# Kernel tuning notes

Measured on AMD Instinct MI355X. Metric: run time of the kernel, lower is better.

## Reference

```python
import jax, jax.numpy as jnp
import numpy as np

B, S, H, L, NH, T, V = 16, 512, 768, 6, 12, 32, 10000


def setup_inputs() -> dict:
    key = jax.random.key(0)
    ks = jax.random.split(key, 16)
    p = lambda i, shape: jax.random.normal(ks[i], shape, jnp.float32) * 0.02
    return {
        "input_ids": jax.random.randint(ks[0], (B, S), 0, V),
        "labels": jax.random.randint(ks[1], (B, S), 0, T),
        "if_crf": 1,
        "emb": p(2, (V, H)),
        "attn_in_w": p(3, (L, 3 * H, H)), "attn_in_b": p(4, (L, 3 * H)),
        "attn_out_w": p(5, (L, H, H)), "attn_out_b": p(6, (L, H)),
        "ln1_g": jnp.ones((L, H), jnp.float32), "ln1_b": jnp.zeros((L, H), jnp.float32),
        "ln2_g": jnp.ones((L, H), jnp.float32), "ln2_b": jnp.zeros((L, H), jnp.float32),
        "ffn_w1": p(7, (L, H, H)), "ffn_b1": p(8, (L, H)),
        "ffn_w2": p(9, (L, H, H)), "ffn_b2": p(10, (L, H)),
        "head_w": p(11, (T, H)), "head_b": p(12, (T,)),
        "crf_start": p(13, (T,)), "crf_end": p(14, (T,)), "crf_trans": p(15, (T, T)),
    }


def _layer_norm(x, g, b, eps=1e-5):
    m = x.mean(-1, keepdims=True)
    v = ((x - m) ** 2).mean(-1, keepdims=True)
    return (x - m) * jax.lax.rsqrt(v + eps) * g + b


def _encoder(x, params):
    # PyTorch post-norm TransformerEncoderLayer, batch_first, relu, dropout=0 (eval)
    def layer(x, p):
        in_w, in_b, out_w, out_b, g1, b1, g2, b2, w1, bb1, w2, bb2 = p
        Bq, Sq, Hq = x.shape
        dh = Hq // NH
        qkv = x @ in_w.T + in_b                       # [B,S,3H]
        q, k, v = jnp.split(qkv, 3, axis=-1)
        q = q.reshape(Bq, Sq, NH, dh).transpose(0, 2, 1, 3)
        k = k.reshape(Bq, Sq, NH, dh).transpose(0, 2, 1, 3)
        v = v.reshape(Bq, Sq, NH, dh).transpose(0, 2, 1, 3)
        scale = 1.0 / np.sqrt(dh).astype(np.float32).item()
        a = jax.nn.softmax(jnp.einsum('bhqd,bhkd->bhqk', q, k) * scale, axis=-1)
        o = jnp.einsum('bhqk,bhkd->bhqd', a, v).transpose(0, 2, 1, 3).reshape(Bq, Sq, Hq)
        o = o @ out_w.T + out_b
        x = _layer_norm(x + o, g1, b1)
        ff = jax.nn.relu(x @ w1.T + bb1) @ w2.T + bb2
        x = _layer_norm(x + ff, g2, b2)
        return x, None
    x, _ = jax.lax.scan(layer, x, params)
    return x


def _crf_llh(emis, tags, start, end, trans):
    # torchcrf log-likelihood, no mask, reduction='sum'
    Bq = emis.shape[0]
    emit = jnp.take_along_axis(emis, tags[:, :, None], axis=2)[:, :, 0].sum(1)   # [B]
    tr = trans[tags[:, :-1], tags[:, 1:]].sum(1)                                 # [B]
    num = start[tags[:, 0]] + emit + tr + end[tags[:, -1]]
    # partition via forward algorithm (scan over time)
    def step(score, e_t):  # score [B,T], e_t [B,T]
        ns = jax.nn.logsumexp(score[:, :, None] + trans[None], axis=1) + e_t
        return ns, None
    score0 = start[None] + emis[:, 0]
    scoreN, _ = jax.lax.scan(step, score0, jnp.swapaxes(emis, 0, 1)[1:])
    logZ = jax.nn.logsumexp(scoreN + end[None], axis=1)
    return (num - logZ).sum()


def _viterbi(emis, start, end, trans):
    score0 = start[None] + emis[:, 0]
    def step(score, e_t):
        cand = score[:, :, None] + trans[None]   # [B,T,T]
        return cand.max(1) + e_t, cand.argmax(1)
    scoreN, hist = jax.lax.scan(step, score0, jnp.swapaxes(emis, 0, 1)[1:])  # hist [S-1,B,T]
    last = (scoreN + end[None]).argmax(1)  # [B]
    def back(tag, h_t):
        prev = jnp.take_along_axis(h_t, tag[:, None], axis=1)[:, 0]
        return prev, prev
    _, prevs = jax.lax.scan(back, last, hist, reverse=True)  # prevs[i] = tag at pos i
    return jnp.concatenate([prevs.T, last[:, None]], axis=1)  # [B,S]


def reference(input_ids, labels, if_crf, emb, attn_in_w, attn_in_b, attn_out_w, attn_out_b,
              ln1_g, ln1_b, ln2_g, ln2_b, ffn_w1, ffn_b1, ffn_w2, ffn_b2,
              head_w, head_b, crf_start, crf_end, crf_trans):
    x = emb[input_ids]
    params = (attn_in_w, attn_in_b, attn_out_w, attn_out_b, ln1_g, ln1_b, ln2_g, ln2_b,
              ffn_w1, ffn_b1, ffn_w2, ffn_b2)
    logits = _encoder(x, params)            # [B,S,H]
    emis = logits @ head_w.T + head_b       # [B,S,T]
    if if_crf:
        llh = _crf_llh(emis, labels, crf_start, crf_end, crf_trans)
        tags = _viterbi(emis, crf_start, crf_end, crf_trans)
        return logits, -llh / 10000.0, tags
    else:
        return logits, emis, jnp.argmax(emis, axis=-1)
```

## Files before the change

### kernel.cpp

```cpp
#include <hip/hip_runtime.h>

#define MTOK 8192
#define HD   768
#define H3   2304
#define NL   6
#define TT   32

typedef __attribute__((ext_vector_type(4))) float f32x4;
typedef __attribute__((ext_vector_type(8))) short v8bf;
typedef __attribute__((ext_vector_type(4))) unsigned short us4;
typedef __attribute__((ext_vector_type(8))) unsigned short us8;

__device__ __forceinline__ unsigned short bf16rne(float v) {
    unsigned int u = __float_as_uint(v);
    u += 0x7FFFu + ((u >> 16) & 1u);
    return (unsigned short)(u >> 16);
}
__device__ __forceinline__ float bf2f(unsigned short h) {
    return __uint_as_float(((unsigned int)h) << 16);
}
__device__ __forceinline__ unsigned int split_pack(float v) {
    unsigned short h = bf16rne(v);
    unsigned short m = bf16rne(v - bf2f(h));
    return (unsigned int)h | ((unsigned int)m << 16);
}

__device__ __forceinline__ void gload16(const unsigned short* g, unsigned short* l) {
    __builtin_amdgcn_global_load_lds(
        (const __attribute__((address_space(1))) unsigned int*)g,
        (__attribute__((address_space(3))) unsigned int*)l, 16, 0, 0);
}

__global__ __launch_bounds__(256)
void wsplit_kernel(const float* __restrict__ src, unsigned short* __restrict__ h,
                   unsigned short* __restrict__ m, int n4)
{
    int i = blockIdx.x * 256 + threadIdx.x;
    if (i >= n4) return;
    float4 v = reinterpret_cast<const float4*>(src)[i];
    us4 hv, mv; unsigned int p;
    p = split_pack(v.x); hv[0] = (unsigned short)p; mv[0] = (unsigned short)(p >> 16);
    p = split_pack(v.y); hv[1] = (unsigned short)p; mv[1] = (unsigned short)(p >> 16);
    p = split_pack(v.z); hv[2] = (unsigned short)p; mv[2] = (unsigned short)(p >> 16);
    p = split_pack(v.w); hv[3] = (unsigned short)p; mv[3] = (unsigned short)(p >> 16);
    reinterpret_cast<us4*>(h)[i] = hv;
    reinterpret_cast<us4*>(m)[i] = mv;
}

template<bool RELU, bool SPLITOUT>
__global__ __launch_bounds__(256)
void gemm_pair_kernel(const unsigned short* __restrict__ Ahg, const unsigned short* __restrict__ Amg,
                      const unsigned short* __restrict__ Bhg, const unsigned short* __restrict__ Bmg,
                      const float* __restrict__ bias, float* __restrict__ Cf,
                      unsigned short* __restrict__ Ch, unsigned short* __restrict__ Cm, int N)
{
    __shared__ unsigned short lds[4][128 * 64];
    const int tid = threadIdx.x;
    const int lane = tid & 63, wave = tid >> 6;
    const int wm = wave >> 1, wn = wave & 1;
    const int bn = blockIdx.x, bm = blockIdx.y;
    const int g = lane >> 4, lr = lane & 15;

    const int srow = lane >> 3;
    const int schunk = ((lane & 7) ^ srow) * 8;
    const size_t aoff = ((size_t)(bm * 128 + wave * 32 + srow)) * HD + schunk;
    const size_t boff = ((size_t)(bn * 128 + wave * 32 + srow)) * HD + schunk;

    f32x4 acc[4][4] = {};

    for (int kt = 0; kt < 12; ++kt) {
        __syncthreads();
        const int k64 = kt * 64;
        #pragma unroll
        for (int i = 0; i < 4; ++i) {
            const size_t ra = aoff + (size_t)i * 8 * HD + k64;
            const size_t rb = boff + (size_t)i * 8 * HD + k64;
            unsigned short* lb = (unsigned short*)&lds[0][(wave * 32 + i * 8) * 64];
            gload16(Ahg + ra, lb);
            gload16(Amg + ra, lb + 8192);
            gload16(Bhg + rb, lb + 16384);
            gload16(Bmg + rb, lb + 24576);
        }
        __syncthreads();
        #pragma unroll
        for (int kk = 0; kk < 2; ++kk) {
            v8bf ah[4], am[4], bh[4], bmv[4];
            #pragma unroll
            for (int i = 0; i < 4; ++i) {
                int row = wm * 64 + i * 16 + lr;
                int ub = row * 64 + ((((kk << 2) + g) ^ (row & 7)) << 3);
                ah[i] = *reinterpret_cast<const v8bf*>(&lds[0][ub]);
                am[i] = *reinterpret_cast<const v8bf*>(&lds[1][ub]);
            }
            #pragma unroll
            for (int i = 0; i < 4; ++i) {
                int row = wn * 64 + i * 16 + lr;
                int ub = row * 64 + ((((kk << 2) + g) ^ (row & 7)) << 3);
                bh[i]  = *reinterpret_cast<const v8bf*>(&lds[2][ub]);
                bmv[i] = *reinterpret_cast<const v8bf*>(&lds[3][ub]);
            }
            #pragma unroll
            for (int i = 0; i < 4; ++i)
                #pragma unroll
                for (int j = 0; j < 4; ++j) {
                    acc[i][j] = __builtin_amdgcn_mfma_f32_16x16x32_bf16(ah[i], bh[j],  acc[i][j], 0, 0, 0);
                    acc[i][j] = __builtin_amdgcn_mfma_f32_16x16x32_bf16(ah[i], bmv[j], acc[i][j], 0, 0, 0);
                    acc[i][j] = __builtin_amdgcn_mfma_f32_16x16x32_bf16(am[i], bh[j],  acc[i][j], 0, 0, 0);
                    acc[i][j] = __builtin_amdgcn_mfma_f32_16x16x32_bf16(am[i], bmv[j], acc[i][j], 0, 0, 0);
                }
        }
    }
    #pragma unroll
    for (int j = 0; j < 4; ++j) {
        int n = bn * 128 + wn * 64 + j * 16 + lr;
        float bv = bias[n];
        #pragma unroll
        for (int i = 0; i < 4; ++i) {
            int mr = bm * 128 + wm * 64 + i * 16 + 4 * g;
            #pragma unroll
            for (int r = 0; r < 4; ++r) {
                float y = acc[i][j][r] + bv;
                if (RELU) y = fmaxf(y, 0.0f);
                size_t idx = (size_t)(mr + r) * N + n;
                if (SPLITOUT) {
                    unsigned int pk = split_pack(y);
                    Ch[idx] = (unsigned short)pk;
                    Cm[idx] = (unsigned short)(pk >> 16);
                } else {
                    Cf[idx] = y;
                }
            }
        }
    }
}

__global__ __launch_bounds__(256)
void vtrans_kernel(const unsigned short* __restrict__ qh, const unsigned short* __restrict__ qm,
                   unsigned short* __restrict__ vth, unsigned short* __restrict__ vtm)
{
    __shared__ unsigned short Th[4096], Tm[4096];
    const int kt = blockIdx.x, bh = blockIdx.y;
    const int b = bh / 12, h = bh % 12;
    const int tid = threadIdx.x;
    #pragma unroll
    for (int is = 0; is < 2; ++is) {
        int c = is * 256 + tid;
        int r = c >> 3, dc = c & 7;
        size_t src = ((size_t)b * 512 + kt * 64 + r) * H3 + 1536 + h * 64 + dc * 8;
        int swz = (dc ^ (r & 7) ^ (r >> 3)) * 8;
        *reinterpret_cast<us8*>(&Th[r * 64 + swz]) = *reinterpret_cast<const us8*>(&qh[src]);
        *reinterpret_cast<us8*>(&Tm[r * 64 + swz]) = *reinterpret_cast<const us8*>(&qm[src]);
    }
    __syncthreads();
    #pragma unroll
    for (int is = 0; is < 2; ++is) {
        int c = is * 256 + tid;
        int d = c >> 3, rg = c & 7;
        us8 vh, vm;
        #pragma unroll
        for (int e = 0; e < 8; ++e) {
            int r = rg * 8 + e;
            int addr = r * 64 + (((d >> 3) ^ (r & 7) ^ (r >> 3)) * 8) + (d & 7);
            vh[e] = Th[addr]; vm[e] = Tm[addr];
        }
        size_t dst = ((size_t)bh * 64 + d) * 512 + kt * 64 + rg * 8;
        *reinterpret_cast<us8*>(&vth[dst]) = vh;
        *reinterpret_cast<us8*>(&vtm[dst]) = vm;
    }
}

__global__ __launch_bounds__(256, 2)
void attn_kernel(const unsigned short* __restrict__ qh, const unsigned short* __restrict__ qm,
                 const unsigned short* __restrict__ vth, const unsigned short* __restrict__ vtm,
                 unsigned short* __restrict__ ohp, unsigned short* __restrict__ omp)
{
    __shared__ unsigned short Kh[4096], Km[4096], Vh[4096], Vm[4096];
    __shared__ unsigned short Ph[4][1024], Pm[4][1024];
    const int qhalf = blockIdx.x;
    const int bh = blockIdx.y;
    const int b = bh / 12, h = bh % 12;
    const int tid = threadIdx.x, lane = tid & 63, wave = tid >> 6;
    const int g = lane >> 4, lr = lane & 15;
    const size_t rowbase = (size_t)b * 512;
    const int qbase = qhalf * 256 + wave * 64;

    v8bf aqh[4][2], aqm[4][2];
    #pragma unroll
    for (int i = 0; i < 4; ++i)
        #pragma unroll
        for (int kk = 0; kk < 2; ++kk) {
            size_t a = (rowbase + qbase + i * 16 + lr) * H3 + h * 64 + (kk * 4 + g) * 8;
            aqh[i][kk] = *reinterpret_cast<const v8bf*>(&qh[a]);
            aqm[i][kk] = *reinterpret_cast<const v8bf*>(&qm[a]);
        }

    float m_run[4][4], l_run[4][4];
    f32x4 O[4][4];
    #pragma unroll
    for (int i = 0; i < 4; ++i)
        #pragma unroll
        for (int r = 0; r < 4; ++r) {
            m_run[i][r] = -__builtin_inff(); l_run[i][r] = 0.0f;
            O[i][r] = (f32x4){0.0f, 0.0f, 0.0f, 0.0f};
        }

    const int srow = lane >> 3;
    const int schunk = ((lane & 7) ^ srow) * 8;

    for (int kt = 0; kt < 8; ++kt) {
        __syncthreads();
        #pragma unroll
        for (int is = 0; is < 2; ++is) {
            int rowg = is * 32 + wave * 8;
            size_t ksrc = (rowbase + kt * 64 + rowg + srow) * H3 + 768 + h * 64 + schunk;
            size_t vsrc = ((size_t)bh * 64 + rowg + srow) * 512 + kt * 64 + schunk;
            gload16(qh + ksrc, &Kh[rowg * 64]);
            gload16(qm + ksrc, &Km[rowg * 64]);
            gload16(vth + vsrc, &Vh[rowg * 64]);
            gload16(vtm + vsrc, &Vm[rowg * 64]);
        }
        __syncthreads();

        #pragma unroll
        for (int i = 0; i < 4; ++i) {
            f32x4 s[4] = {};
            #pragma unroll
            for (int kk = 0; kk < 2; ++kk) {
                #pragma unroll
                for (int j = 0; j < 4; ++j) {
                    int krow = j * 16 + lr;
                    int uk = krow * 64 + (((kk * 4 + g) ^ (krow & 7)) * 8);
                    v8bf bkh = *reinterpret_cast<const v8bf*>(&Kh[uk]);
                    v8bf bkm = *reinterpret_cast<const v8bf*>(&Km[uk]);
                    s[j] = __builtin_amdgcn_mfma_f32_16x16x32_bf16(aqh[i][kk], bkh, s[j], 0, 0, 0);
                    s[j] = __builtin_amdgcn_mfma_f32_16x16x32_bf16(aqh[i][kk], bkm, s[j], 0, 0, 0);
                    s[j] = __builtin_amdgcn_mfma_f32_16x16x32_bf16(aqm[i][kk], bkh, s[j], 0, 0, 0);
                }
            }
            float mnew[4], alpha[4], rsum[4];
            #pragma unroll
            for (int rr = 0; rr < 4; ++rr) {
                float t = fmaxf(fmaxf(s[0][rr], s[1][rr]), fmaxf(s[2][rr], s[3][rr])) * 0.125f;
                #pragma unroll
                for (int off = 1; off < 16; off <<= 1) t = fmaxf(t, __shfl_xor(t, off));
                mnew[rr] = fmaxf(m_run[i][rr], t);
                alpha[rr] = __expf(m_run[i][rr] - mnew[rr]);
                m_run[i][rr] = mnew[rr];
                rsum[rr] = 0.0f;
            }
            #pragma unroll
            for (int j = 0; j < 4; ++j) {
                #pragma unroll
                for (int rr = 0; rr < 4; ++rr) {
                    float p = __expf(s[j][rr] * 0.125f - mnew[rr]);
                    rsum[rr] += p;
                    int prow = 4 * g + rr;
                    int ub = prow * 64 + ((((j * 2 + (lr >> 3)) ^ (prow & 7)) << 3) | (lr & 7));
                    unsigned int pk = split_pack(p);
                    Ph[wave][ub] = (unsigned short)pk; Pm[wave][ub] = (unsigned short)(pk >> 16);
                }
            }
            #pragma unroll
            for (int rr = 0; rr < 4; ++rr) {
                float t = rsum[rr];
                #pragma unroll
                for (int off = 1; off < 16; off <<= 1) t += __shfl_xor(t, off);
                l_run[i][rr] = l_run[i][rr] * alpha[rr] + t;
                O[i][0][rr] *= alpha[rr]; O[i][1][rr] *= alpha[rr];
                O[i][2][rr] *= alpha[rr]; O[i][3][rr] *= alpha[rr];
            }
            #pragma unroll
            for (int kk = 0; kk < 2; ++kk) {
                int up = lr * 64 + (((kk * 4 + g) ^ (lr & 7)) * 8);
                v8bf aph = *reinterpret_cast<const v8bf*>(&Ph[wave][up]);
                v8bf apm = *reinterpret_cast<const v8bf*>(&Pm[wave][up]);
                #pragma unroll
                for (int j = 0; j < 4; ++j) {
                    int vrow = j * 16 + lr;
                    int uv = vrow * 64 + (((kk * 4 + g) ^ (vrow & 7)) * 8);
                    v8bf bvh = *reinterpret_cast<const v8bf*>(&Vh[uv]);
                    v8bf bvm = *reinterpret_cast<const v8bf*>(&Vm[uv]);
                    O[i][j] = __builtin_amdgcn_mfma_f32_16x16x32_bf16(aph, bvh, O[i][j], 0, 0, 0);
                    O[i][j] = __builtin_amdgcn_mfma_f32_16x16x32_bf16(aph, bvm, O[i][j], 0, 0, 0);
                    O[i][j] = __builtin_amdgcn_mfma_f32_16x16x32_bf16(apm, bvh, O[i][j], 0, 0, 0);
                }
            }
        }
    }
    #pragma unroll
    for (int i = 0; i < 4; ++i)
        #pragma unroll
        for (int j = 0; j < 4; ++j) {
            int d = j * 16 + lr;
            #pragma unroll
            for (int rr = 0; rr < 4; ++rr) {
                size_t tok = rowbase + qbase + i * 16 + 4 * g + rr;
                unsigned int pk = split_pack(O[i][j][rr] / l_run[i][rr]);
                ohp[tok * HD + h * 64 + d] = (unsigned short)pk;
                omp[tok * HD + h * 64 + d] = (unsigned short)(pk >> 16);
            }
        }
}

__global__ __launch_bounds__(256)
void ln_residual_kernel(unsigned short* __restrict__ xh, unsigned short* __restrict__ xm,
                        const float* __restrict__ t,
                        const float* __restrict__ gamma, const float* __restrict__ beta)
{
    int tok = blockIdx.x * 4 + (threadIdx.x >> 6);
    int lane = threadIdx.x & 63;
    float v[12];
    float s = 0.0f;
    #pragma unroll
    for (int j = 0; j < 12; ++j) {
        size_t c = (size_t)tok * HD + j * 64 + lane;
        v[j] = bf2f(xh[c]) + bf2f(xm[c]) + t[c];
        s += v[j];
    }
    #pragma unroll
    for (int off = 32; off; off >>= 1) s += __shfl_xor(s, off);
    float mean = s * (1.0f / 768.0f);
    float vs = 0.0f;
    #pragma unroll
    for (int j = 0; j < 12; ++j) { float d = v[j] - mean; vs += d * d; }
    #pragma unroll
    for (int off = 32; off; off >>= 1) vs += __shfl_xor(vs, off);
    float rstd = rsqrtf(vs * (1.0f / 768.0f) + 1e-5f);
    #pragma unroll
    for (int j = 0; j < 12; ++j) {
        size_t c = (size_t)tok * HD + j * 64 + lane;
        float y = (v[j] - mean) * rstd * gamma[j * 64 + lane] + beta[j * 64 + lane];
        unsigned int pk = split_pack(y);
        xh[c] = (unsigned short)pk; xm[c] = (unsigned short)(pk >> 16);
    }
}

__global__ __launch_bounds__(256)
void embed_kernel(const int* __restrict__ ids, const float* __restrict__ emb,
                  unsigned short* __restrict__ xh, unsigned short* __restrict__ xm)
{
    int f4 = blockIdx.x * 256 + threadIdx.x;
    int tok = f4 / 192, c = f4 % 192;
    float4 v = *reinterpret_cast<const float4*>(emb + (size_t)ids[tok] * HD + c * 4);
    us4 hv, mv; unsigned int p;
    p = split_pack(v.x); hv[0] = (unsigned short)p; mv[0] = (unsigned short)(p >> 16);
    p = split_pack(v.y); hv[1] = (unsigned short)p; mv[1] = (unsigned short)(p >> 16);
    p = split_pack(v.z); hv[2] = (unsigned short)p; mv[2] = (unsigned short)(p >> 16);
    p = split_pack(v.w); hv[3] = (unsigned short)p; mv[3] = (unsigned short)(p >> 16);
    *reinterpret_cast<us4*>(&xh[(size_t)tok * HD + c * 4]) = hv;
    *reinterpret_cast<us4*>(&xm[(size_t)tok * HD + c * 4]) = mv;
}

__global__ __launch_bounds__(256)
void out_logits_kernel(const unsigned short* __restrict__ xh, const unsigned short* __restrict__ xm,
                       float* __restrict__ out)
{
    int i = blockIdx.x * 256 + threadIdx.x;
    us4 hv = reinterpret_cast<const us4*>(xh)[i];
    us4 mv = reinterpret_cast<const us4*>(xm)[i];
    float4 o;
    o.x = bf2f(hv[0]) + bf2f(mv[0]);
    o.y = bf2f(hv[1]) + bf2f(mv[1]);
    o.z = bf2f(hv[2]) + bf2f(mv[2]);
    o.w = bf2f(hv[3]) + bf2f(mv[3]);
    reinterpret_cast<float4*>(out)[i] = o;
}

__global__ __launch_bounds__(256)
void emis_kernel(const unsigned short* __restrict__ xh, const unsigned short* __restrict__ xm,
                 const float* __restrict__ hw, const float* __restrict__ hb,
                 float* __restrict__ emis)
{
    int tok = blockIdx.x * 4 + (threadIdx.x >> 6);
    int lane = threadIdx.x & 63;
    float xv[12];
    #pragma unroll
    for (int j = 0; j < 12; ++j) {
        size_t c = (size_t)tok * HD + j * 64 + lane;
        xv[j] = bf2f(xh[c]) + bf2f(xm[c]);
    }
    for (int t = 0; t < TT; ++t) {
        float a = 0.0f;
        #pragma unroll
        for (int j = 0; j < 12; ++j) a += xv[j] * hw[t * HD + j * 64 + lane];
        #pragma unroll
        for (int off = 32; off; off >>= 1) a += __shfl_xor(a, off);
        if (lane == 0) emis[(size_t)tok * TT + t] = a + hb[t];
    }
}

__global__ void crf_num_kernel(const float* __restrict__ emis, const int* __restrict__ labels,
                               const float* __restrict__ start, const float* __restrict__ end,
                               const float* __restrict__ trans, float* __restrict__ num)
{
    int b = blockIdx.x, lane = threadIdx.x;
    float a = 0.0f;
    for (int s = lane; s < 512; s += 64) {
        int lab = labels[b * 512 + s];
        a += emis[(size_t)(b * 512 + s) * TT + lab];
        if (s > 0) a += trans[labels[b * 512 + s - 1] * TT + lab];
        else a += start[lab];
        if (s == 511) a += end[lab];
    }
    #pragma unroll
    for (int off = 32; off; off >>= 1) a += __shfl_xor(a, off);
    if (lane == 0) num[b] = a;
}

__global__ __launch_bounds__(64)
void crf_path_kernel(const float* __restrict__ emis, const float* __restrict__ start,
                     const float* __restrict__ end, const float* __restrict__ trans,
                     float* __restrict__ logZ, float* __restrict__ out_tags)
{
    const int mode = blockIdx.x >> 4;
    const int b = blockIdx.x & 15;
    const int lane = threadIdx.x;
    const int j = lane & 31;
    const int h = lane >> 5;
    const int hbase = h << 4;
    __shared__ unsigned char hist[511][32];
    __shared__ float sval[32];
    __shared__ int path[512];

    const float* eb = emis + (size_t)b * 512 * TT;

    float cur[8], nxt[8];
    #pragma unroll
    for (int i = 0; i < 8; ++i) cur[i] = eb[(1 + i) * TT + j];

    if (mode == 0) {
        float Ecol[16];
        #pragma unroll
        for (int ii = 0; ii < 16; ++ii) Ecol[ii] = __expf(trans[(hbase + ii) * TT + j]);
        float sc = start[j] + eb[j];
        for (int base = 1; base < 512; base += 8) {
            #pragma unroll
            for (int i = 0; i < 8; ++i) {
                int s = base + 8 + i;
                nxt[i] = eb[(s < 512 ? s : 511) * TT + j];
            }
            #pragma unroll
            for (int i = 0; i < 8; ++i) {
                if (base + i < 512) {
                    float r = __shfl(sc, 0);
                    float p = __expf(sc - r);
                    float dot = 0.0f;
                    #pragma unroll
                    for (int ii = 0; ii < 16; ++ii)
                        dot = fmaf(__shfl(p, hbase + ii), Ecol[ii], dot);
                    dot += __shfl_xor(dot, 32);
                    sc = r + __logf(dot) + cur[i];
                }
            }
            #pragma unroll
            for (int i = 0; i < 8; ++i) cur[i] = nxt[i];
        }
        float v = sc + end[j];
        float mx = v;
        #pragma unroll
        for (int off = 1; off < 32; off <<= 1) mx = fmaxf(mx, __shfl_xor(mx, off));
        float p = __expf(v - mx);
        float sm = p;
        #pragma unroll
        for (int off = 1; off < 32; off <<= 1) sm += __shfl_xor(sm, off);
        if (lane == 0) logZ[b] = mx + __logf(sm);
    } else {
        float tcol[16];
        #pragma unroll
        for (int ii = 0; ii < 16; ++ii) tcol[ii] = trans[(hbase + ii) * TT + j];
        float sc = start[j] + eb[j];
        for (int base = 1; base < 512; base += 8) {
            #pragma unroll
            for (int i = 0; i < 8; ++i) {
                int s = base + 8 + i;
                nxt[i] = eb[(s < 512 ? s : 511) * TT + j];
            }
            #pragma unroll
            for (int i = 0; i < 8; ++i) {
                if (base + i < 512) {
                    int s = base + i;
                    float best = __shfl(sc, hbase) + tcol[0];
                    int arg = hbase;
                    #pragma unroll
                    for (int ii = 1; ii < 16; ++ii) {
                        float c = __shfl(sc, hbase + ii) + tcol[ii];
                        if (c > best) { best = c; arg = hbase + ii; }
                    }
                    float vo = __shfl_xor(best, 32);
                    int   ao = __shfl_xor(arg, 32);
                    bool take = h ? !(best > vo) : (vo > best);
                    if (take) { best = vo; arg = ao; }
                    if (h == 0) hist[s - 1][j] = (unsigned char)arg;
                    sc = best + cur[i];
                }
            }
            #pragma unroll
            for (int i = 0; i < 8; ++i) cur[i] = nxt[i];
        }
        if (h == 0) sval[j] = sc + end[j];
        __syncthreads();
        if (lane == 0) {
            float best = sval[0]; int arg = 0;
            for (int i = 1; i < TT; ++i)
                if (sval[i] > best) { best = sval[i]; arg = i; }
            int t = arg; path[511] = t;
            for (int s = 510; s >= 0; --s) { t = hist[s][t]; path[s] = t; }
        }
        __syncthreads();
        for (int s = lane; s < 512; s += 64)
            out_tags[(size_t)b * 512 + s] = (float)path[s];
    }
}

__global__ void crf_loss_kernel(const float* __restrict__ num, const float* __restrict__ logZ,
                                float* __restrict__ out)
{
    if (threadIdx.x == 0) {
        float s = 0.0f;
        for (int b = 0; b < 16; ++b) s += num[b] - logZ[b];
        out[0] = -s / 10000.0f;
    }
}

extern "C" void kernel_launch(void* const* d_in, const int* in_sizes, int n_in,
                              void* d_out, int out_size, void* d_ws, size_t ws_size,
                              hipStream_t stream)
{
    (void)in_sizes; (void)n_in; (void)out_size; (void)ws_size;
    const int*   input_ids = (const int*)d_in[0];
    const int*   labels    = (const int*)d_in[1];
    const float* emb   = (const float*)d_in[3];
    const float* in_w  = (const float*)d_in[4];
    const float* in_b  = (const float*)d_in[5];
    const float* out_w = (const float*)d_in[6];
    const float* out_b = (const float*)d_in[7];
    const float* ln1g  = (const float*)d_in[8];
    const float* ln1b  = (const float*)d_in[9];
    const float* ln2g  = (const float*)d_in[10];
    const float* ln2b  = (const float*)d_in[11];
    const float* w1    = (const float*)d_in[12];
    const float* b1    = (const float*)d_in[13];
    const float* w2    = (const float*)d_in[14];
    const float* b2    = (const float*)d_in[15];
    const float* hw    = (const float*)d_in[16];
    const float* hb    = (const float*)d_in[17];
    const float* cs    = (const float*)d_in[18];
    const float* ce    = (const float*)d_in[19];
    const float* ct    = (const float*)d_in[20];
    float* out = (float*)d_out;

    char* ws = (char*)d_ws;
    unsigned short* xh   = (unsigned short*)(ws);
    unsigned short* xm   = (unsigned short*)(ws + 12582912);
    unsigned short* qkvh = (unsigned short*)(ws + 25165824);
    unsigned short* qkvm = (unsigned short*)(ws + 62914560);
    unsigned short* ohb  = (unsigned short*)(ws + 100663296);
    unsigned short* omb  = (unsigned short*)(ws + 113246208);
    float*          tmp  = (float*)(ws + 125829120);
    unsigned short* vth  = (unsigned short*)(ws + 125829120);
    unsigned short* vtm  = (unsigned short*)(ws + 138412032);
    unsigned short* wih  = (unsigned short*)(ws + 150994944);
    unsigned short* wim  = (unsigned short*)(ws + 154533888);
    unsigned short* woh  = (unsigned short*)(ws + 158072832);
    unsigned short* wom  = (unsigned short*)(ws + 159252480);
    unsigned short* w1h  = (unsigned short*)(ws + 160432128);
    unsigned short* w1m  = (unsigned short*)(ws + 161611776);
    unsigned short* w2h  = (unsigned short*)(ws + 162791424);
    unsigned short* w2m  = (unsigned short*)(ws + 163971072);
    unsigned short* f1h  = qkvh;
    unsigned short* f1m  = qkvm;
    float* emis = (float*)(ws + 100663296);
    float* numb = (float*)(ws + 100663296 + 1048576);
    float* logZ = numb + 16;

    embed_kernel<<<MTOK * 192 / 256, 256, 0, stream>>>(input_ids, emb, xh, xm);

    for (int l = 0; l < NL; ++l) {
        wsplit_kernel<<<1728, 256, 0, stream>>>(in_w + (size_t)l * H3 * HD, wih, wim, H3 * HD / 4);
        wsplit_kernel<<<576, 256, 0, stream>>>(out_w + (size_t)l * HD * HD, woh, wom, HD * HD / 4);
        wsplit_kernel<<<576, 256, 0, stream>>>(w1 + (size_t)l * HD * HD, w1h, w1m, HD * HD / 4);
        wsplit_kernel<<<576, 256, 0, stream>>>(w2 + (size_t)l * HD * HD, w2h, w2m, HD * HD / 4);

        gemm_pair_kernel<false, true><<<dim3(18, 64), 256, 0, stream>>>(
            xh, xm, wih, wim, in_b + (size_t)l * H3, nullptr, qkvh, qkvm, H3);
        vtrans_kernel<<<dim3(8, 192), 256, 0, stream>>>(qkvh, qkvm, vth, vtm);
        attn_kernel<<<dim3(2, 192), 256, 0, stream>>>(qkvh, qkvm, vth, vtm, ohb, omb);
        gemm_pair_kernel<false, false><<<dim3(6, 64), 256, 0, stream>>>(
            ohb, omb, woh, wom, out_b + (size_t)l * HD, tmp, nullptr, nullptr, HD);
        ln_residual_kernel<<<2048, 256, 0, stream>>>(xh, xm, tmp, ln1g + l * HD, ln1b + l * HD);
        gemm_pair_kernel<true, true><<<dim3(6, 64), 256, 0, stream>>>(
            xh, xm, w1h, w1m, b1 + (size_t)l * HD, nullptr, f1h, f1m, HD);
        gemm_pair_kernel<false, false><<<dim3(6, 64), 256, 0, stream>>>(
            f1h, f1m, w2h, w2m, b2 + (size_t)l * HD, tmp, nullptr, nullptr, HD);
        ln_residual_kernel<<<2048, 256, 0, stream>>>(xh, xm, tmp, ln2g + l * HD, ln2b + l * HD);
    }

    out_logits_kernel<<<MTOK * 192 / 256, 256, 0, stream>>>(xh, xm, out);

    emis_kernel<<<2048, 256, 0, stream>>>(xh, xm, hw, hb, emis);
    crf_num_kernel<<<16, 64, 0, stream>>>(emis, labels, cs, ce, ct, numb);
    crf_path_kernel<<<32, 64, 0, stream>>>(emis, cs, ce, ct, logZ, out + 6291457);
    crf_loss_kernel<<<1, 64, 0, stream>>>(numb, logZ, out + 6291456);
}
```

Measured before the change: 2.580 ms.

## Drop low-low split product, merge weight splits, rework CRF scans to 32 lanes

Result: faster. 2.360 ms (-8.5%).

```diff
diff --git a/kernel.cpp b/kernel.cpp
--- a/kernel.cpp
+++ b/kernel.cpp
@@ -32,19 +32,27 @@
 }
 
 __global__ __launch_bounds__(256)
-void wsplit_kernel(const float* __restrict__ src, unsigned short* __restrict__ h,
-                   unsigned short* __restrict__ m, int n4)
+void wsplit4_kernel(const float* __restrict__ inw, const float* __restrict__ outw,
+                    const float* __restrict__ w1, const float* __restrict__ w2,
+                    unsigned short* __restrict__ wih, unsigned short* __restrict__ wim,
+                    unsigned short* __restrict__ woh, unsigned short* __restrict__ wom,
+                    unsigned short* __restrict__ w1h, unsigned short* __restrict__ w1m,
+                    unsigned short* __restrict__ w2h, unsigned short* __restrict__ w2m)
 {
     int i = blockIdx.x * 256 + threadIdx.x;
-    if (i >= n4) return;
-    float4 v = reinterpret_cast<const float4*>(src)[i];
+    const float* src; unsigned short* dh; unsigned short* dm; int off;
+    if (i < 442368)      { src = inw;  dh = wih; dm = wim; off = i; }
+    else if (i < 589824) { src = outw; dh = woh; dm = wom; off = i - 442368; }
+    else if (i < 737280) { src = w1;   dh = w1h; dm = w1m; off = i - 589824; }
+    else                 { src = w2;   dh = w2h; dm = w2m; off = i - 737280; }
+    float4 v = reinterpret_cast<const float4*>(src)[off];
     us4 hv, mv; unsigned int p;
     p = split_pack(v.x); hv[0] = (unsigned short)p; mv[0] = (unsigned short)(p >> 16);
     p = split_pack(v.y); hv[1] = (unsigned short)p; mv[1] = (unsigned short)(p >> 16);
     p = split_pack(v.z); hv[2] = (unsigned short)p; mv[2] = (unsigned short)(p >> 16);
     p = split_pack(v.w); hv[3] = (unsigned short)p; mv[3] = (unsigned short)(p >> 16);
-    reinterpret_cast<us4*>(h)[i] = hv;
-    reinterpret_cast<us4*>(m)[i] = mv;
+    reinterpret_cast<us4*>(dh)[off] = hv;
+    reinterpret_cast<us4*>(dm)[off] = mv;
 }
 
 template<bool RELU, bool SPLITOUT>
@@ -106,7 +114,6 @@
                     acc[i][j] = __builtin_amdgcn_mfma_f32_16x16x32_bf16(ah[i], bh[j],  acc[i][j], 0, 0, 0);
                     acc[i][j] = __builtin_amdgcn_mfma_f32_16x16x32_bf16(ah[i], bmv[j], acc[i][j], 0, 0, 0);
                     acc[i][j] = __builtin_amdgcn_mfma_f32_16x16x32_bf16(am[i], bh[j],  acc[i][j], 0, 0, 0);
-                    acc[i][j] = __builtin_amdgcn_mfma_f32_16x16x32_bf16(am[i], bmv[j], acc[i][j], 0, 0, 0);
                 }
         }
     }
@@ -416,88 +423,108 @@
     const int b = blockIdx.x & 15;
     const int lane = threadIdx.x;
     const int j = lane & 31;
-    const int h = lane >> 5;
-    const int hbase = h << 4;
+    __shared__ float xch[32];
     __shared__ unsigned char hist[511][32];
     __shared__ float sval[32];
     __shared__ int path[512];
 
     const float* eb = emis + (size_t)b * 512 * TT;
 
-    float cur[8], nxt[8];
-    #pragma unroll
-    for (int i = 0; i < 8; ++i) cur[i] = eb[(1 + i) * TT + j];
-
     if (mode == 0) {
-        float Ecol[16];
-        #pragma unroll
-        for (int ii = 0; ii < 16; ++ii) Ecol[ii] = __expf(trans[(hbase + ii) * TT + j]);
-        float sc = start[j] + eb[j];
-        for (int base = 1; base < 512; base += 8) {
-            #pragma unroll
-            for (int i = 0; i < 8; ++i) {
-                int s = base + 8 + i;
-                nxt[i] = eb[(s < 512 ? s : 511) * TT + j];
-            }
-            #pragma unroll
-            for (int i = 0; i < 8; ++i) {
-                if (base + i < 512) {
-                    float r = __shfl(sc, 0);
-                    float p = __expf(sc - r);
-                    float dot = 0.0f;
-                    #pragma unroll
-                    for (int ii = 0; ii < 16; ++ii)
-                        dot = fmaf(__shfl(p, hbase + ii), Ecol[ii], dot);
-                    dot += __shfl_xor(dot, 32);
-                    sc = r + __logf(dot) + cur[i];
-                }
-            }
-            #pragma unroll
-            for (int i = 0; i < 8; ++i) cur[i] = nxt[i];
-        }
-        float v = sc + end[j];
-        float mx = v;
-        #pragma unroll
-        for (int off = 1; off < 32; off <<= 1) mx = fmaxf(mx, __shfl_xor(mx, off));
-        float p = __expf(v - mx);
-        float sm = p;
-        #pragma unroll
-        for (int off = 1; off < 32; off <<= 1) sm += __shfl_xor(sm, off);
-        if (lane == 0) logZ[b] = mx + __logf(sm);
+        if (lane < 32) {
+            float Ecol[32];
+            #pragma unroll
+            for (int ii = 0; ii < 32; ++ii) Ecol[ii] = __expf(trans[ii * TT + j]);
+            float cur[8], nxt[8];
+            #pragma unroll
+            for (int i = 0; i < 8; ++i) cur[i] = eb[(1 + i) * TT + j];
+            float sc = start[j] + eb[j];
+            for (int base = 1; base < 512; base += 8) {
+                #pragma unroll
+                for (int i = 0; i < 8; ++i) {
+                    int s = base + 8 + i;
+                    nxt[i] = eb[(s < 512 ? s : 511) * TT + j];
+                }
+                #pragma unroll
+                for (int i = 0; i < 8; ++i) {
+                    if (base + i < 512) {
+                        xch[j] = sc;
+                        asm volatile("s_waitcnt lgkmcnt(0)" ::: "memory");
+                        float r = xch[0];
+                        float p = __expf(sc - r);
+                        asm volatile("" ::: "memory");
+                        xch[j] = p;
+                        asm volatile("s_waitcnt lgkmcnt(0)" ::: "memory");
+                        float dot = 0.0f;
+                        #pragma unroll
+                        for (int q = 0; q < 8; ++q) {
+                            f32x4 t4 = *reinterpret_cast<const f32x4*>(&xch[q * 4]);
+                            dot = fmaf(t4[0], Ecol[q * 4 + 0], dot);
+                            dot = fmaf(t4[1], Ecol[q * 4 + 1], dot);
+                            dot = fmaf(t4[2], Ecol[q * 4 + 2], dot);
+                            dot = fmaf(t4[3], Ecol[q * 4 + 3], dot);
+                        }
+                        asm volatile("" ::: "memory");
+                        sc = r + __logf(dot) + cur[i];
+                    }
+                }
+                #pragma unroll
+                for (int i = 0; i < 8; ++i) cur[i] = nxt[i];
+            }
+            float v = sc + end[j];
+            float mx = v;
+            #pragma unroll
+            for (int off = 1; off < 32; off <<= 1) mx = fmaxf(mx, __shfl_xor(mx, off));
+            float p = __expf(v - mx);
+            float sm = p;
+            #pragma unroll
+            for (int off = 1; off < 32; off <<= 1) sm += __shfl_xor(sm, off);
+            if (lane == 0) logZ[b] = mx + __logf(sm);
+        }
     } else {
-        float tcol[16];
-        #pragma unroll
-        for (int ii = 0; ii < 16; ++ii) tcol[ii] = trans[(hbase + ii) * TT + j];
-        float sc = start[j] + eb[j];
-        for (int base = 1; base < 512; base += 8) {
-            #pragma unroll
-            for (int i = 0; i < 8; ++i) {
-                int s = base + 8 + i;
-                nxt[i] = eb[(s < 512 ? s : 511) * TT + j];
-            }
-            #pragma unroll
-            for (int i = 0; i < 8; ++i) {
-                if (base + i < 512) {
-                    int s = base + i;
-                    float best = __shfl(sc, hbase) + tcol[0];
-                    int arg = hbase;
-                    #pragma unroll
-                    for (int ii = 1; ii < 16; ++ii) {
-                        float c = __shfl(sc, hbase + ii) + tcol[ii];
-                        if (c > best) { best = c; arg = hbase + ii; }
+        if (lane < 32) {
+            float tcol[32];
+            #pragma unroll
+            for (int ii = 0; ii < 32; ++ii) tcol[ii] = trans[ii * TT + j];
+            float cur[8], nxt[8];
+            #pragma unroll
+            for (int i = 0; i < 8; ++i) cur[i] = eb[(1 + i) * TT + j];
+            float sc = start[j] + eb[j];
+            for (int base = 1; base < 512; base += 8) {
+                #pragma unroll
+                for (int i = 0; i < 8; ++i) {
+                    int s = base + 8 + i;
+                    nxt[i] = eb[(s < 512 ? s : 511) * TT + j];
+                }
+                #pragma unroll
+                for (int i = 0; i < 8; ++i) {
+                    if (base + i < 512) {
+                        int s = base + i;
+                        xch[j] = sc;
+                        asm volatile("s_waitcnt lgkmcnt(0)" ::: "memory");
+                        float c[32];
+                        #pragma unroll
+                        for (int q = 0; q < 8; ++q) {
+                            f32x4 t4 = *reinterpret_cast<const f32x4*>(&xch[q * 4]);
+                            c[q * 4 + 0] = t4[0] + tcol[q * 4 + 0];
+                            c[q * 4 + 1] = t4[1] + tcol[q * 4 + 1];
+                            c[q * 4 + 2] = t4[2] + tcol[q * 4 + 2];
+                            c[q * 4 + 3] = t4[3] + tcol[q * 4 + 3];
+                        }
+                        asm volatile("" ::: "memory");
+                        float best = c[0]; int arg = 0;
+                        #pragma unroll
+                        for (int ii = 1; ii < 32; ++ii)
+                            if (c[ii] > best) { best = c[ii]; arg = ii; }
+                        hist[s - 1][j] = (unsigned char)arg;
+                        sc = best + cur[i];
                     }
-                    float vo = __shfl_xor(best, 32);
-                    int   ao = __shfl_xor(arg, 32);
-                    bool take = h ? !(best > vo) : (vo > best);
-                    if (take) { best = vo; arg = ao; }
-                    if (h == 0) hist[s - 1][j] = (unsigned char)arg;
-                    sc = best + cur[i];
-                }
-            }
-            #pragma unroll
-            for (int i = 0; i < 8; ++i) cur[i] = nxt[i];
-        }
-        if (h == 0) sval[j] = sc + end[j];
+                }
+                #pragma unroll
+                for (int i = 0; i < 8; ++i) cur[i] = nxt[i];
+            }
+            sval[j] = sc + end[j];
+        }
         __syncthreads();
         if (lane == 0) {
             float best = sval[0]; int arg = 0;
@@ -576,10 +603,10 @@
     embed_kernel<<<MTOK * 192 / 256, 256, 0, stream>>>(input_ids, emb, xh, xm);
 
     for (int l = 0; l < NL; ++l) {
-        wsplit_kernel<<<1728, 256, 0, stream>>>(in_w + (size_t)l * H3 * HD, wih, wim, H3 * HD / 4);
-        wsplit_kernel<<<576, 256, 0, stream>>>(out_w + (size_t)l * HD * HD, woh, wom, HD * HD / 4);
-        wsplit_kernel<<<576, 256, 0, stream>>>(w1 + (size_t)l * HD * HD, w1h, w1m, HD * HD / 4);
-        wsplit_kernel<<<576, 256, 0, stream>>>(w2 + (size_t)l * HD * HD, w2h, w2m, HD * HD / 4);
+        wsplit4_kernel<<<3456, 256, 0, stream>>>(
+            in_w + (size_t)l * H3 * HD, out_w + (size_t)l * HD * HD,
+            w1 + (size_t)l * HD * HD, w2 + (size_t)l * HD * HD,
+            wih, wim, woh, wom, w1h, w1m, w2h, w2m);
 
         gemm_pair_kernel<false, true><<<dim3(18, 64), 256, 0, stream>>>(
             xh, xm, wih, wim, in_b + (size_t)l * H3, nullptr, qkvh, qkvm, H3);
```
